# Optimization experiments

Measured on AMD Instinct MI355X. Metric: run time of the kernel, lower is better.

The kernel has to match this reference:

```python
import jax, jax.numpy as jnp
import numpy as np

B, T, H, F, K, NB, MAXL = 32, 512, 512, 512, 3, 256, 2048


def _conv1d(x, w, b, pad):
    # x: [B,T,Cin], w: [K,Cin,Cout] -> [B,T,Cout]
    y = jax.lax.conv_general_dilated(x, w, window_strides=(1,), padding=[(pad, pad)],
                                     dimension_numbers=('NWC', 'WIO', 'NWC'))
    return y + b


def _layernorm(x, g, b):
    m = jnp.mean(x, axis=-1, keepdims=True)
    v = jnp.mean((x - m) ** 2, axis=-1, keepdims=True)
    return (x - m) * jax.lax.rsqrt(v + 1e-5) * g + b


def _variance_predictor(x, mask, cw1, cb1, g1, b1, cw2, cb2, g2, b2, lw, lb, k):
    # ConvNorm(k, pad=(k-1)//2) -> ReLU -> LN -> ConvNorm(k, pad=1) -> ReLU -> LN -> Linear(F,1)
    h = _layernorm(jax.nn.relu(_conv1d(x, cw1, cb1, (k - 1) // 2)), g1, b1)
    h = _layernorm(jax.nn.relu(_conv1d(h, cw2, cb2, 1)), g2, b2)
    out = h @ lw + lb  # [B,T]
    return jnp.where(mask, 0.0, out)


def setup_inputs() -> dict:
    key = jax.random.key(0)
    ks = jax.random.split(key, 12)
    s = 0.02
    inp = {
        'x': jax.random.normal(ks[0], (B, T, H), jnp.float32),
        'src_mask': jnp.zeros((B, T), jnp.bool_),
        'duration': jax.random.randint(ks[1], (B, T), 0, 8),
        'pitch_target': jax.random.normal(ks[2], (B, T), jnp.float32),
        'energy_target': jax.random.normal(ks[3], (B, T), jnp.float32),
        # stacked predictor params: index 0=duration, 1=pitch, 2=energy
        'conv1_w': jax.random.normal(ks[4], (3, K, H, F), jnp.float32) * s,
        'conv1_b': jnp.zeros((3, F), jnp.float32),
        'ln1_g': jnp.ones((3, F), jnp.float32),
        'ln1_b': jnp.zeros((3, F), jnp.float32),
        'conv2_w': jax.random.normal(ks[5], (3, K, F, F), jnp.float32) * s,
        'conv2_b': jnp.zeros((3, F), jnp.float32),
        'ln2_g': jnp.ones((3, F), jnp.float32),
        'ln2_b': jnp.zeros((3, F), jnp.float32),
        'lin_w': jax.random.normal(ks[6], (3, F), jnp.float32) * s,
        'lin_b': jnp.zeros((3,), jnp.float32),
        'pitch_bins': jnp.linspace(-3.0, 3.0, NB - 1, dtype=jnp.float32),
        'energy_bins': jnp.linspace(-3.0, 3.0, NB - 1, dtype=jnp.float32),
        'pitch_table': jax.random.normal(ks[7], (NB, H), jnp.float32) * s,
        'energy_table': jax.random.normal(ks[8], (NB, H), jnp.float32) * s,
        'max_len': MAXL,
    }
    return inp


def reference(x, src_mask, duration, pitch_target, energy_target,
              conv1_w, conv1_b, ln1_g, ln1_b, conv2_w, conv2_b, ln2_g, ln2_b,
              lin_w, lin_b, pitch_bins, energy_bins, pitch_table, energy_table, max_len):
    k = conv1_w.shape[1]

    def vp(i, inp):
        return _variance_predictor(inp, src_mask, conv1_w[i], conv1_b[i], ln1_g[i], ln1_b[i],
                                   conv2_w[i], conv2_b[i], ln2_g[i], ln2_b[i], lin_w[i], lin_b[i], k)

    log_duration_pred = vp(0, x)
    # pitch: predict, bucketize target, add embedding (training path with targets)
    pitch_pred = vp(1, x)
    p_idx = jnp.searchsorted(pitch_bins, pitch_target)  # torch.bucketize
    x = x + pitch_table[p_idx]
    # energy on pitch-conditioned features
    energy_pred = vp(2, x)
    e_idx = jnp.searchsorted(energy_bins, energy_target)
    x = x + energy_table[e_idx]

    # LengthRegulator: expand each phoneme vec duration[b,i] times, pad to max_len
    dur = jnp.where(src_mask, 0, duration)
    cum = jnp.cumsum(dur, axis=1)                 # [B,T]
    mel_len = jnp.minimum(cum[:, -1], max_len)    # [B]
    frames = jnp.arange(max_len)
    idx = jax.vmap(lambda c: jnp.searchsorted(c, frames, side='right'))(cum)
    idx = jnp.clip(idx, 0, x.shape[1] - 1)        # [B,max_len]
    x_out = jnp.take_along_axis(x, idx[:, :, None], axis=1)  # [B,max_len,H]
    mel_mask = frames[None, :] >= mel_len[:, None]
    x_out = jnp.where(mel_mask[:, :, None], 0.0, x_out)
    return x_out, log_duration_pred, pitch_pred, energy_pred, mel_len, mel_mask
```

## Files before the change

kernel.cpp:

```cpp
#include <hip/hip_runtime.h>
#include <hip/hip_bf16.h>

typedef unsigned short ushort_t;
typedef unsigned int uint_t;
typedef __attribute__((ext_vector_type(8))) short bf16x8;
typedef __attribute__((ext_vector_type(4))) float f32x4;

#define NB_T 512
#define NB_H 512
#define NB_B 32
#define NB_M (NB_B * NB_T)
#define KDIM 1536
#define MAXL 2048

__device__ __forceinline__ ushort_t f2bf(float f) {
  __hip_bfloat16 h = __float2bfloat16(f);
  return *reinterpret_cast<ushort_t*>(&h);
}
__device__ __forceinline__ float bf2f(ushort_t u) {
  __hip_bfloat16 h;
  *reinterpret_cast<ushort_t*>(&h) = u;
  return __bfloat162float(h);
}
__device__ __forceinline__ uint_t pack2(float a, float b) {
  return (uint_t)f2bf(a) | ((uint_t)f2bf(b) << 16);
}
__device__ __forceinline__ void gload_lds16(const void* g, void* l) {
  __builtin_amdgcn_global_load_lds((const __attribute__((address_space(1))) void*)g,
                                   (__attribute__((address_space(3))) void*)l, 16, 0, 0);
}

__global__ __launch_bounds__(256) void k_wt(const float* __restrict__ w, ushort_t* __restrict__ wt) {
  __shared__ float tile[64][65];
  const int pk = blockIdx.y;
  const int p = pk / 3, kk = pk % 3;
  const int ot = (blockIdx.x & 7) * 64;
  const int it = (blockIdx.x >> 3) * 64;
  const int tx = threadIdx.x & 63;
  const int ty = threadIdx.x >> 6;
  const float* src = w + (size_t)pk * 512 * 512;
  #pragma unroll
  for (int r = ty; r < 64; r += 4)
    tile[r][tx] = src[(size_t)(it + r) * 512 + ot + tx];
  __syncthreads();
  #pragma unroll
  for (int r = ty; r < 64; r += 4)
    wt[((size_t)(p * 512 + ot + r)) * KDIM + kk * 512 + it + tx] = f2bf(tile[tx][r]);
}

__global__ __launch_bounds__(256) void k_prep_x(const float* __restrict__ x,
                                                ushort_t* __restrict__ xb_pad,
                                                ushort_t* __restrict__ ln_pad) {
  const int rp = blockIdx.x;
  const int b = rp / 514, j = rp % 514;
  const int tid = threadIdx.x;
  uint_t* dstA = (uint_t*)(xb_pad + (size_t)rp * 512);
  if (j == 0 || j == 513) {
    dstA[tid] = 0u;
    ((uint_t*)(ln_pad + (size_t)rp * 512))[tid] = 0u;
  } else {
    const float2 xv = ((const float2*)(x + ((size_t)(b * NB_T + j - 1)) * 512))[tid];
    dstA[tid] = pack2(xv.x, xv.y);
  }
}

__global__ __launch_bounds__(256) void k_bucket(const float* __restrict__ pt, const float* __restrict__ et,
                                                const float* __restrict__ pb, const float* __restrict__ eb,
                                                int* __restrict__ pi, int* __restrict__ ei) {
  const int i = blockIdx.x * 256 + threadIdx.x;
  if (i >= NB_M) return;
  float v = pt[i];
  int lo = 0, hi = 255;
  while (lo < hi) { int mid = (lo + hi) >> 1; if (pb[mid] < v) lo = mid + 1; else hi = mid; }
  pi[i] = lo;
  v = et[i]; lo = 0; hi = 255;
  while (lo < hi) { int mid = (lo + hi) >> 1; if (eb[mid] < v) lo = mid + 1; else hi = mid; }
  ei[i] = lo;
}

__global__ __launch_bounds__(512) void k_cum(const int* __restrict__ dur, const unsigned char* __restrict__ mask,
                                             int* __restrict__ cum, float* __restrict__ mel_len_out,
                                             float* __restrict__ mel_mask_out) {
  __shared__ int s[512];
  const int b = blockIdx.x, t = threadIdx.x;
  int d = mask[b * NB_T + t] ? 0 : dur[b * NB_T + t];
  s[t] = d;
  __syncthreads();
  for (int off = 1; off < 512; off <<= 1) {
    int v = (t >= off) ? s[t - off] : 0;
    __syncthreads();
    s[t] += v;
    __syncthreads();
  }
  cum[b * NB_T + t] = s[t];
  int ml = s[511]; ml = ml < MAXL ? ml : MAXL;
  if (t == 0) mel_len_out[b] = (float)ml;
  for (int f = t; f < MAXL; f += 512)
    mel_mask_out[b * MAXL + f] = (f >= ml) ? 1.0f : 0.0f;
}

__global__ __launch_bounds__(256) void k_gemm(const ushort_t* __restrict__ Apad,
                                              const ushort_t* __restrict__ Wt,
                                              const float* __restrict__ bias,
                                              ushort_t* __restrict__ H) {
  __shared__ short lA[128 * 32];
  __shared__ short lB[128 * 32];
  const int tid = threadIdx.x;
  const int lane = tid & 63, wid = tid >> 6;
  const int mt = blockIdx.x >> 2, nt = blockIdx.x & 3;
  const int m0 = mt * 128, n0 = nt * 128;
  const int b = m0 >> 9, t0 = m0 & 511;
  const long Arow0 = (long)b * 514 + t0 + 1;

  const int subr = lane >> 2;
  const int ioff = (lane & 3) * 8;

  f32x4 acc[4][4];
  #pragma unroll
  for (int i = 0; i < 4; ++i)
    #pragma unroll
    for (int j = 0; j < 4; ++j) acc[i][j] = (f32x4)0.f;

  const int wr = wid >> 1, wc = wid & 1;
  const int lr = lane & 15, kg = lane >> 4;

  for (int kk = 0; kk < 48; ++kk) {
    const int dt = (kk >> 4) - 1;
    const int i0 = (kk & 15) << 5;
    #pragma unroll
    for (int q = 0; q < 2; ++q) {
      const int chunk = wid * 2 + q;
      const int r = chunk * 16 + subr;
      const ushort_t* gsrc = Apad + (size_t)(Arow0 + r + dt) * 512 + i0 + ioff;
      gload_lds16(gsrc, &lA[chunk * 512]);
    }
    #pragma unroll
    for (int q = 0; q < 2; ++q) {
      const int chunk = wid * 2 + q;
      const int r = chunk * 16 + subr;
      const ushort_t* gsrc = Wt + (size_t)(n0 + r) * KDIM + kk * 32 + ioff;
      gload_lds16(gsrc, &lB[chunk * 512]);
    }
    __syncthreads();
    bf16x8 af[4], bfv[4];
    #pragma unroll
    for (int fi = 0; fi < 4; ++fi)
      af[fi] = *(const bf16x8*)&lA[(wr * 64 + fi * 16 + lr) * 32 + kg * 8];
    #pragma unroll
    for (int fj = 0; fj < 4; ++fj)
      bfv[fj] = *(const bf16x8*)&lB[(wc * 64 + fj * 16 + lr) * 32 + kg * 8];
    #pragma unroll
    for (int fi = 0; fi < 4; ++fi)
      #pragma unroll
      for (int fj = 0; fj < 4; ++fj)
        acc[fi][fj] = __builtin_amdgcn_mfma_f32_16x16x32_bf16(af[fi], bfv[fj], acc[fi][fj], 0, 0, 0);
    __syncthreads();
  }

  #pragma unroll
  for (int fi = 0; fi < 4; ++fi) {
    const int row = m0 + wr * 64 + fi * 16 + kg * 4;
    #pragma unroll
    for (int fj = 0; fj < 4; ++fj) {
      const int col = n0 + wc * 64 + fj * 16 + lr;
      const float bv = bias[col];
      #pragma unroll
      for (int r = 0; r < 4; ++r) {
        float v = acc[fi][fj][r] + bv;
        v = v > 0.f ? v : 0.f;
        H[(size_t)(row + r) * 512 + col] = f2bf(v);
      }
    }
  }
}

__global__ __launch_bounds__(256) void k_ln_mid(const ushort_t* __restrict__ Hh,
                                                const float* __restrict__ g, const float* __restrict__ bb,
                                                ushort_t* __restrict__ out_pad) {
  const int row = blockIdx.x * 4 + (threadIdx.x >> 6);
  const int lane = threadIdx.x & 63;
  bf16x8 v = *(const bf16x8*)(Hh + (size_t)row * 512 + lane * 8);
  float xv[8];
  float s = 0.f;
  #pragma unroll
  for (int j = 0; j < 8; ++j) { xv[j] = bf2f((ushort_t)v[j]); s += xv[j]; }
  #pragma unroll
  for (int m = 32; m >= 1; m >>= 1) s += __shfl_xor(s, m, 64);
  const float mean = s * (1.f / 512.f);
  float vs = 0.f;
  #pragma unroll
  for (int j = 0; j < 8; ++j) { float d = xv[j] - mean; vs += d * d; }
  #pragma unroll
  for (int m = 32; m >= 1; m >>= 1) vs += __shfl_xor(vs, m, 64);
  const float rstd = rsqrtf(vs * (1.f / 512.f) + 1e-5f);
  const float4 g0 = ((const float4*)(g + lane * 8))[0];
  const float4 g1 = ((const float4*)(g + lane * 8))[1];
  const float4 b0 = ((const float4*)(bb + lane * 8))[0];
  const float4 b1 = ((const float4*)(bb + lane * 8))[1];
  const float gg[8] = {g0.x, g0.y, g0.z, g0.w, g1.x, g1.y, g1.z, g1.w};
  const float bv[8] = {b0.x, b0.y, b0.z, b0.w, b1.x, b1.y, b1.z, b1.w};
  bf16x8 o;
  #pragma unroll
  for (int j = 0; j < 8; ++j) o[j] = (short)f2bf((xv[j] - mean) * rstd * gg[j] + bv[j]);
  const int bidx = row >> 9, t = row & 511;
  *(bf16x8*)(out_pad + ((size_t)(bidx * 514 + t + 1)) * 512 + lane * 8) = o;
}

__global__ __launch_bounds__(256) void k_ln_fin(const ushort_t* __restrict__ Hh,
                                                const float* __restrict__ g, const float* __restrict__ bb,
                                                const float* __restrict__ lw, const float* __restrict__ lbp,
                                                const unsigned char* __restrict__ mask,
                                                float* __restrict__ outp) {
  const int row = blockIdx.x * 4 + (threadIdx.x >> 6);
  const int lane = threadIdx.x & 63;
  bf16x8 v = *(const bf16x8*)(Hh + (size_t)row * 512 + lane * 8);
  float xv[8];
  float s = 0.f;
  #pragma unroll
  for (int j = 0; j < 8; ++j) { xv[j] = bf2f((ushort_t)v[j]); s += xv[j]; }
  #pragma unroll
  for (int m = 32; m >= 1; m >>= 1) s += __shfl_xor(s, m, 64);
  const float mean = s * (1.f / 512.f);
  float vs = 0.f;
  #pragma unroll
  for (int j = 0; j < 8; ++j) { float d = xv[j] - mean; vs += d * d; }
  #pragma unroll
  for (int m = 32; m >= 1; m >>= 1) vs += __shfl_xor(vs, m, 64);
  const float rstd = rsqrtf(vs * (1.f / 512.f) + 1e-5f);
  const float4 g0 = ((const float4*)(g + lane * 8))[0];
  const float4 g1 = ((const float4*)(g + lane * 8))[1];
  const float4 b0 = ((const float4*)(bb + lane * 8))[0];
  const float4 b1 = ((const float4*)(bb + lane * 8))[1];
  const float4 w0 = ((const float4*)(lw + lane * 8))[0];
  const float4 w1 = ((const float4*)(lw + lane * 8))[1];
  const float gg[8] = {g0.x, g0.y, g0.z, g0.w, g1.x, g1.y, g1.z, g1.w};
  const float bv[8] = {b0.x, b0.y, b0.z, b0.w, b1.x, b1.y, b1.z, b1.w};
  const float ww[8] = {w0.x, w0.y, w0.z, w0.w, w1.x, w1.y, w1.z, w1.w};
  float dot = 0.f;
  #pragma unroll
  for (int j = 0; j < 8; ++j) dot += ((xv[j] - mean) * rstd * gg[j] + bv[j]) * ww[j];
  #pragma unroll
  for (int m = 32; m >= 1; m >>= 1) dot += __shfl_xor(dot, m, 64);
  if (lane == 0) {
    float val = dot + lbp[0];
    if (mask[row]) val = 0.f;
    outp[row] = val;
  }
}

__global__ __launch_bounds__(256) void k_addemb1(const float* __restrict__ x, const float* __restrict__ tab,
                                                 const int* __restrict__ idx, float* __restrict__ x2f,
                                                 ushort_t* __restrict__ xb_pad) {
  const int m = blockIdx.x, tid = threadIdx.x;
  const int b = m >> 9, t = m & 511;
  const float2 xv = ((const float2*)(x + (size_t)m * 512))[tid];
  const float2 tv = ((const float2*)(tab + (size_t)idx[m] * 512))[tid];
  float2 r; r.x = xv.x + tv.x; r.y = xv.y + tv.y;
  ((float2*)(x2f + (size_t)m * 512))[tid] = r;
  ((uint_t*)(xb_pad + ((size_t)(b * 514 + t + 1)) * 512))[tid] = pack2(r.x, r.y);
}

__global__ __launch_bounds__(256) void k_addemb2(const float* __restrict__ tab, const int* __restrict__ idx,
                                                 float* __restrict__ x2f) {
  const int m = blockIdx.x, tid = threadIdx.x;
  const float2 tv = ((const float2*)(tab + (size_t)idx[m] * 512))[tid];
  float2 r = ((const float2*)(x2f + (size_t)m * 512))[tid];
  r.x += tv.x; r.y += tv.y;
  ((float2*)(x2f + (size_t)m * 512))[tid] = r;
}

__global__ __launch_bounds__(128) void k_regulate(const float* __restrict__ x2f, const int* __restrict__ cum,
                                                  float* __restrict__ xout) {
  const int bid = blockIdx.x;
  const int b = bid >> 11, f = bid & 2047;
  const int* c = cum + b * NB_T;
  int ml = c[511]; ml = ml < MAXL ? ml : MAXL;
  const int tid = threadIdx.x;
  float4 val = make_float4(0.f, 0.f, 0.f, 0.f);
  if (f < ml) {
    int lo = 0, hi = 512;
    while (lo < hi) { int mid = (lo + hi) >> 1; if (c[mid] <= f) lo = mid + 1; else hi = mid; }
    if (lo > 511) lo = 511;
    val = ((const float4*)(x2f + ((size_t)(b * NB_T + lo)) * 512))[tid];
  }
  ((float4*)(xout + ((size_t)(b * MAXL + f)) * 512))[tid] = val;
}

extern "C" void kernel_launch(void* const* d_in, const int* in_sizes, int n_in,
                              void* d_out, int out_size, void* d_ws, size_t ws_size,
                              hipStream_t stream) {
  const float* x        = (const float*)d_in[0];
  const unsigned char* src_mask = (const unsigned char*)d_in[1];
  const int* duration   = (const int*)d_in[2];
  const float* pitch_t  = (const float*)d_in[3];
  const float* energy_t = (const float*)d_in[4];
  const float* conv1_w  = (const float*)d_in[5];
  const float* conv1_b  = (const float*)d_in[6];
  const float* ln1_g    = (const float*)d_in[7];
  const float* ln1_b    = (const float*)d_in[8];
  const float* conv2_w  = (const float*)d_in[9];
  const float* conv2_b  = (const float*)d_in[10];
  const float* ln2_g    = (const float*)d_in[11];
  const float* ln2_b    = (const float*)d_in[12];
  const float* lin_w    = (const float*)d_in[13];
  const float* lin_b    = (const float*)d_in[14];
  const float* pbins    = (const float*)d_in[15];
  const float* ebins    = (const float*)d_in[16];
  const float* ptab     = (const float*)d_in[17];
  const float* etab     = (const float*)d_in[18];

  char* ws = (char*)d_ws;
  ushort_t* xb_pad = (ushort_t*)(ws + 0);
  ushort_t* ln_pad = (ushort_t*)(ws + 16842752);
  ushort_t* wt1    = (ushort_t*)(ws + 33685504);
  ushort_t* wt2    = (ushort_t*)(ws + 38404096);
  ushort_t* hbuf   = (ushort_t*)(ws + 43122688);
  float*    x2f    = (float*)   (ws + 59899904);
  int*      p_idx  = (int*)     (ws + 93454336);
  int*      e_idx  = (int*)     (ws + 93519872);
  int*      cum    = (int*)     (ws + 93585408);

  float* out      = (float*)d_out;
  float* o_xout   = out;
  float* o_logd   = out + 33554432;
  float* o_pitch  = o_logd + 16384;
  float* o_energy = o_pitch + 16384;
  float* o_mellen = o_energy + 16384;
  float* o_mmask  = o_mellen + 32;

  k_wt<<<dim3(64, 9), 256, 0, stream>>>(conv1_w, wt1);
  k_wt<<<dim3(64, 9), 256, 0, stream>>>(conv2_w, wt2);
  k_prep_x<<<NB_B * 514, 256, 0, stream>>>(x, xb_pad, ln_pad);
  k_bucket<<<NB_M / 256, 256, 0, stream>>>(pitch_t, energy_t, pbins, ebins, p_idx, e_idx);
  k_cum<<<NB_B, 512, 0, stream>>>(duration, src_mask, cum, o_mellen, o_mmask);

  k_gemm<<<512, 256, 0, stream>>>(xb_pad, wt1, conv1_b, hbuf);
  k_ln_mid<<<NB_M / 4, 256, 0, stream>>>(hbuf, ln1_g, ln1_b, ln_pad);
  k_gemm<<<512, 256, 0, stream>>>(ln_pad, wt2, conv2_b, hbuf);
  k_ln_fin<<<NB_M / 4, 256, 0, stream>>>(hbuf, ln2_g, ln2_b, lin_w, lin_b, src_mask, o_logd);

  k_gemm<<<512, 256, 0, stream>>>(xb_pad, wt1 + (size_t)1 * 512 * KDIM, conv1_b + 512, hbuf);
  k_ln_mid<<<NB_M / 4, 256, 0, stream>>>(hbuf, ln1_g + 512, ln1_b + 512, ln_pad);
  k_gemm<<<512, 256, 0, stream>>>(ln_pad, wt2 + (size_t)1 * 512 * KDIM, conv2_b + 512, hbuf);
  k_ln_fin<<<NB_M / 4, 256, 0, stream>>>(hbuf, ln2_g + 512, ln2_b + 512, lin_w + 512, lin_b + 1, src_mask, o_pitch);

  k_addemb1<<<NB_M, 256, 0, stream>>>(x, ptab, p_idx, x2f, xb_pad);

  k_gemm<<<512, 256, 0, stream>>>(xb_pad, wt1 + (size_t)2 * 512 * KDIM, conv1_b + 1024, hbuf);
  k_ln_mid<<<NB_M / 4, 256, 0, stream>>>(hbuf, ln1_g + 1024, ln1_b + 1024, ln_pad);
  k_gemm<<<512, 256, 0, stream>>>(ln_pad, wt2 + (size_t)2 * 512 * KDIM, conv2_b + 1024, hbuf);
  k_ln_fin<<<NB_M / 4, 256, 0, stream>>>(hbuf, ln2_g + 1024, ln2_b + 1024, lin_w + 1024, lin_b + 2, src_mask, o_energy);

  k_addemb2<<<NB_M, 256, 0, stream>>>(etab, e_idx, x2f);

  k_regulate<<<NB_B * MAXL, 128, 0, stream>>>(x2f, cum, o_xout);
}
```

Before: 573.0 us.

## Batch three predictors into single GEMM/LN launches with double-buffered LDS and staged epilogue

Runs the duration, pitch and energy predictors together. Each GEMM and LayerNorm stage becomes one launch over all three predictors instead of three sequential launches. Both embedding additions move up front into a single prep kernel that also builds the padded bf16 inputs. The GEMM now double-buffers its LDS tiles so the next K-slice load overlaps the MFMAs, remaps blocks with a swizzle, and stages its output through LDS for vectorized stores. In exchange it uses more workspace, since there are three padded input buffers and a hidden buffer three times larger, and it reuses the layer-1 input buffers in place as the layer-2 inputs.

```diff
diff --git a/kernel.cpp b/kernel.cpp
--- a/kernel.cpp
+++ b/kernel.cpp
@@ -7,11 +7,11 @@
 typedef __attribute__((ext_vector_type(4))) float f32x4;
 
 #define NB_T 512
-#define NB_H 512
 #define NB_B 32
 #define NB_M (NB_B * NB_T)
 #define KDIM 1536
 #define MAXL 2048
+#define EPI_STRIDE 144
 
 __device__ __forceinline__ ushort_t f2bf(float f) {
   __hip_bfloat16 h = __float2bfloat16(f);
@@ -46,22 +46,6 @@
   #pragma unroll
   for (int r = ty; r < 64; r += 4)
     wt[((size_t)(p * 512 + ot + r)) * KDIM + kk * 512 + it + tx] = f2bf(tile[tx][r]);
-}
-
-__global__ __launch_bounds__(256) void k_prep_x(const float* __restrict__ x,
-                                                ushort_t* __restrict__ xb_pad,
-                                                ushort_t* __restrict__ ln_pad) {
-  const int rp = blockIdx.x;
-  const int b = rp / 514, j = rp % 514;
-  const int tid = threadIdx.x;
-  uint_t* dstA = (uint_t*)(xb_pad + (size_t)rp * 512);
-  if (j == 0 || j == 513) {
-    dstA[tid] = 0u;
-    ((uint_t*)(ln_pad + (size_t)rp * 512))[tid] = 0u;
-  } else {
-    const float2 xv = ((const float2*)(x + ((size_t)(b * NB_T + j - 1)) * 512))[tid];
-    dstA[tid] = pack2(xv.x, xv.y);
-  }
 }
 
 __global__ __launch_bounds__(256) void k_bucket(const float* __restrict__ pt, const float* __restrict__ et,
@@ -99,111 +83,165 @@
     mel_mask_out[b * MAXL + f] = (f >= ml) ? 1.0f : 0.0f;
 }
 
-__global__ __launch_bounds__(256) void k_gemm(const ushort_t* __restrict__ Apad,
+__global__ __launch_bounds__(256) void k_prep(const float* __restrict__ x,
+                                              const float* __restrict__ ptab, const float* __restrict__ etab,
+                                              const int* __restrict__ pidx, const int* __restrict__ eidx,
+                                              ushort_t* __restrict__ xb_pad, ushort_t* __restrict__ x2pad,
+                                              ushort_t* __restrict__ lnp2, float* __restrict__ x3f) {
+  const int rp = blockIdx.x;
+  const int b = rp / 514, j = rp % 514;
+  const int tid = threadIdx.x;
+  if (j == 0 || j == 513) {
+    ((uint_t*)(xb_pad + (size_t)rp * 512))[tid] = 0u;
+    ((uint_t*)(x2pad + (size_t)rp * 512))[tid] = 0u;
+    ((uint_t*)(lnp2 + (size_t)rp * 512))[tid] = 0u;
+    return;
+  }
+  const int m = b * NB_T + j - 1;
+  const float2 xv = ((const float2*)(x + (size_t)m * 512))[tid];
+  const float2 pv = ((const float2*)(ptab + (size_t)pidx[m] * 512))[tid];
+  const float2 ev = ((const float2*)(etab + (size_t)eidx[m] * 512))[tid];
+  ((uint_t*)(xb_pad + (size_t)rp * 512))[tid] = pack2(xv.x, xv.y);
+  const float ax = xv.x + pv.x, ay = xv.y + pv.y;
+  ((uint_t*)(x2pad + (size_t)rp * 512))[tid] = pack2(ax, ay);
+  float2 o; o.x = ax + ev.x; o.y = ay + ev.y;
+  ((float2*)(x3f + (size_t)m * 512))[tid] = o;
+}
+
+__global__ __launch_bounds__(256) void k_gemm(const ushort_t* __restrict__ A0,
+                                              const ushort_t* __restrict__ A1,
+                                              const ushort_t* __restrict__ A2,
                                               const ushort_t* __restrict__ Wt,
                                               const float* __restrict__ bias,
                                               ushort_t* __restrict__ H) {
-  __shared__ short lA[128 * 32];
-  __shared__ short lB[128 * 32];
+  __shared__ short smem[18432];
   const int tid = threadIdx.x;
   const int lane = tid & 63, wid = tid >> 6;
-  const int mt = blockIdx.x >> 2, nt = blockIdx.x & 3;
+
+  const int h = blockIdx.x;
+  const int logical = (h & 7) * 192 + (h >> 3);
+  const int pred = logical >> 9;
+  const int tile = logical & 511;
+  const int mt = tile >> 2, nt = tile & 3;
   const int m0 = mt * 128, n0 = nt * 128;
   const int b = m0 >> 9, t0 = m0 & 511;
   const long Arow0 = (long)b * 514 + t0 + 1;
 
+  const ushort_t* Ap = (pred == 0) ? A0 : ((pred == 1) ? A1 : A2);
+  const ushort_t* Wp = Wt + (size_t)pred * 512 * KDIM;
+  const float* bp = bias + pred * 512;
+  ushort_t* Hp = H + (size_t)pred * NB_M * 512;
+
   const int subr = lane >> 2;
   const int ioff = (lane & 3) * 8;
-
-  f32x4 acc[4][4];
-  #pragma unroll
-  for (int i = 0; i < 4; ++i)
-    #pragma unroll
-    for (int j = 0; j < 4; ++j) acc[i][j] = (f32x4)0.f;
-
   const int wr = wid >> 1, wc = wid & 1;
   const int lr = lane & 15, kg = lane >> 4;
 
-  for (int kk = 0; kk < 48; ++kk) {
+  f32x4 acc[4][4];
+  #pragma unroll
+  for (int i = 0; i < 4; ++i)
+    #pragma unroll
+    for (int j = 0; j < 4; ++j) acc[i][j] = (f32x4)0.f;
+
+  auto STAGE = [&](int kk, int buf) {
     const int dt = (kk >> 4) - 1;
     const int i0 = (kk & 15) << 5;
+    short* la = &smem[buf * 8192];
+    short* lb = &smem[buf * 8192 + 4096];
     #pragma unroll
     for (int q = 0; q < 2; ++q) {
       const int chunk = wid * 2 + q;
       const int r = chunk * 16 + subr;
-      const ushort_t* gsrc = Apad + (size_t)(Arow0 + r + dt) * 512 + i0 + ioff;
-      gload_lds16(gsrc, &lA[chunk * 512]);
+      gload_lds16(Ap + (size_t)(Arow0 + r + dt) * 512 + i0 + ioff, &la[chunk * 512]);
+      gload_lds16(Wp + (size_t)(n0 + r) * KDIM + kk * 32 + ioff, &lb[chunk * 512]);
     }
-    #pragma unroll
-    for (int q = 0; q < 2; ++q) {
-      const int chunk = wid * 2 + q;
-      const int r = chunk * 16 + subr;
-      const ushort_t* gsrc = Wt + (size_t)(n0 + r) * KDIM + kk * 32 + ioff;
-      gload_lds16(gsrc, &lB[chunk * 512]);
-    }
-    __syncthreads();
+  };
+
+  STAGE(0, 0);
+  __syncthreads();
+  int buf = 0;
+  for (int kk = 0; kk < 48; ++kk) {
+    if (kk < 47) STAGE(kk + 1, buf ^ 1);
+    const short* la = &smem[buf * 8192];
+    const short* lb = &smem[buf * 8192 + 4096];
     bf16x8 af[4], bfv[4];
     #pragma unroll
     for (int fi = 0; fi < 4; ++fi)
-      af[fi] = *(const bf16x8*)&lA[(wr * 64 + fi * 16 + lr) * 32 + kg * 8];
+      af[fi] = *(const bf16x8*)&la[(wr * 64 + fi * 16 + lr) * 32 + kg * 8];
     #pragma unroll
     for (int fj = 0; fj < 4; ++fj)
-      bfv[fj] = *(const bf16x8*)&lB[(wc * 64 + fj * 16 + lr) * 32 + kg * 8];
+      bfv[fj] = *(const bf16x8*)&lb[(wc * 64 + fj * 16 + lr) * 32 + kg * 8];
     #pragma unroll
     for (int fi = 0; fi < 4; ++fi)
       #pragma unroll
       for (int fj = 0; fj < 4; ++fj)
         acc[fi][fj] = __builtin_amdgcn_mfma_f32_16x16x32_bf16(af[fi], bfv[fj], acc[fi][fj], 0, 0, 0);
     __syncthreads();
-  }
-
+    buf ^= 1;
+  }
+
+  float bvv[4];
+  #pragma unroll
+  for (int fj = 0; fj < 4; ++fj) bvv[fj] = bp[n0 + wc * 64 + fj * 16 + lr];
   #pragma unroll
   for (int fi = 0; fi < 4; ++fi) {
-    const int row = m0 + wr * 64 + fi * 16 + kg * 4;
+    const int rowb = wr * 64 + fi * 16 + kg * 4;
     #pragma unroll
     for (int fj = 0; fj < 4; ++fj) {
-      const int col = n0 + wc * 64 + fj * 16 + lr;
-      const float bv = bias[col];
+      const int col = wc * 64 + fj * 16 + lr;
       #pragma unroll
       for (int r = 0; r < 4; ++r) {
-        float v = acc[fi][fj][r] + bv;
+        float v = acc[fi][fj][r] + bvv[fj];
         v = v > 0.f ? v : 0.f;
-        H[(size_t)(row + r) * 512 + col] = f2bf(v);
+        smem[(rowb + r) * EPI_STRIDE + col] = (short)f2bf(v);
       }
     }
   }
+  __syncthreads();
+  #pragma unroll
+  for (int s = 0; s < 8; ++s) {
+    const int chunk = tid + s * 256;
+    const int row = chunk >> 4, c8 = (chunk & 15) * 8;
+    bf16x8 vv = *(const bf16x8*)&smem[row * EPI_STRIDE + c8];
+    *(bf16x8*)(Hp + (size_t)(m0 + row) * 512 + n0 + c8) = vv;
+  }
 }
 
 __global__ __launch_bounds__(256) void k_ln_mid(const ushort_t* __restrict__ Hh,
                                                 const float* __restrict__ g, const float* __restrict__ bb,
-                                                ushort_t* __restrict__ out_pad) {
-  const int row = blockIdx.x * 4 + (threadIdx.x >> 6);
+                                                ushort_t* __restrict__ lnp0, ushort_t* __restrict__ lnp1,
+                                                ushort_t* __restrict__ lnp2) {
+  const int rr = blockIdx.x * 4 + (threadIdx.x >> 6);
+  const int pred = rr >> 14, m = rr & (NB_M - 1);
   const int lane = threadIdx.x & 63;
-  bf16x8 v = *(const bf16x8*)(Hh + (size_t)row * 512 + lane * 8);
+  const float* gp = g + pred * 512;
+  const float* bp = bb + pred * 512;
+  ushort_t* dst = (pred == 0) ? lnp0 : ((pred == 1) ? lnp1 : lnp2);
+  bf16x8 v = *(const bf16x8*)(Hh + (size_t)rr * 512 + lane * 8);
   float xv[8];
   float s = 0.f;
   #pragma unroll
   for (int j = 0; j < 8; ++j) { xv[j] = bf2f((ushort_t)v[j]); s += xv[j]; }
   #pragma unroll
-  for (int m = 32; m >= 1; m >>= 1) s += __shfl_xor(s, m, 64);
+  for (int mm = 32; mm >= 1; mm >>= 1) s += __shfl_xor(s, mm, 64);
   const float mean = s * (1.f / 512.f);
   float vs = 0.f;
   #pragma unroll
   for (int j = 0; j < 8; ++j) { float d = xv[j] - mean; vs += d * d; }
   #pragma unroll
-  for (int m = 32; m >= 1; m >>= 1) vs += __shfl_xor(vs, m, 64);
+  for (int mm = 32; mm >= 1; mm >>= 1) vs += __shfl_xor(vs, mm, 64);
   const float rstd = rsqrtf(vs * (1.f / 512.f) + 1e-5f);
-  const float4 g0 = ((const float4*)(g + lane * 8))[0];
-  const float4 g1 = ((const float4*)(g + lane * 8))[1];
-  const float4 b0 = ((const float4*)(bb + lane * 8))[0];
-  const float4 b1 = ((const float4*)(bb + lane * 8))[1];
+  const float4 g0 = ((const float4*)(gp + lane * 8))[0];
+  const float4 g1 = ((const float4*)(gp + lane * 8))[1];
+  const float4 b0 = ((const float4*)(bp + lane * 8))[0];
+  const float4 b1 = ((const float4*)(bp + lane * 8))[1];
   const float gg[8] = {g0.x, g0.y, g0.z, g0.w, g1.x, g1.y, g1.z, g1.w};
   const float bv[8] = {b0.x, b0.y, b0.z, b0.w, b1.x, b1.y, b1.z, b1.w};
   bf16x8 o;
   #pragma unroll
   for (int j = 0; j < 8; ++j) o[j] = (short)f2bf((xv[j] - mean) * rstd * gg[j] + bv[j]);
-  const int bidx = row >> 9, t = row & 511;
-  *(bf16x8*)(out_pad + ((size_t)(bidx * 514 + t + 1)) * 512 + lane * 8) = o;
+  const int bidx = m >> 9, t = m & 511;
+  *(bf16x8*)(dst + ((size_t)(bidx * 514 + t + 1)) * 512 + lane * 8) = o;
 }
 
 __global__ __launch_bounds__(256) void k_ln_fin(const ushort_t* __restrict__ Hh,
@@ -211,28 +249,32 @@
                                                 const float* __restrict__ lw, const float* __restrict__ lbp,
                                                 const unsigned char* __restrict__ mask,
                                                 float* __restrict__ outp) {
-  const int row = blockIdx.x * 4 + (threadIdx.x >> 6);
+  const int rr = blockIdx.x * 4 + (threadIdx.x >> 6);
+  const int pred = rr >> 14, m = rr & (NB_M - 1);
   const int lane = threadIdx.x & 63;
-  bf16x8 v = *(const bf16x8*)(Hh + (size_t)row * 512 + lane * 8);
+  const float* gp = g + pred * 512;
+  const float* bp = bb + pred * 512;
+  const float* wp = lw + pred * 512;
+  bf16x8 v = *(const bf16x8*)(Hh + (size_t)rr * 512 + lane * 8);
   float xv[8];
   float s = 0.f;
   #pragma unroll
   for (int j = 0; j < 8; ++j) { xv[j] = bf2f((ushort_t)v[j]); s += xv[j]; }
   #pragma unroll
-  for (int m = 32; m >= 1; m >>= 1) s += __shfl_xor(s, m, 64);
+  for (int mm = 32; mm >= 1; mm >>= 1) s += __shfl_xor(s, mm, 64);
   const float mean = s * (1.f / 512.f);
   float vs = 0.f;
   #pragma unroll
   for (int j = 0; j < 8; ++j) { float d = xv[j] - mean; vs += d * d; }
   #pragma unroll
-  for (int m = 32; m >= 1; m >>= 1) vs += __shfl_xor(vs, m, 64);
+  for (int mm = 32; mm >= 1; mm >>= 1) vs += __shfl_xor(vs, mm, 64);
   const float rstd = rsqrtf(vs * (1.f / 512.f) + 1e-5f);
-  const float4 g0 = ((const float4*)(g + lane * 8))[0];
-  const float4 g1 = ((const float4*)(g + lane * 8))[1];
-  const float4 b0 = ((const float4*)(bb + lane * 8))[0];
-  const float4 b1 = ((const float4*)(bb + lane * 8))[1];
-  const float4 w0 = ((const float4*)(lw + lane * 8))[0];
-  const float4 w1 = ((const float4*)(lw + lane * 8))[1];
+  const float4 g0 = ((const float4*)(gp + lane * 8))[0];
+  const float4 g1 = ((const float4*)(gp + lane * 8))[1];
+  const float4 b0 = ((const float4*)(bp + lane * 8))[0];
+  const float4 b1 = ((const float4*)(bp + lane * 8))[1];
+  const float4 w0 = ((const float4*)(wp + lane * 8))[0];
+  const float4 w1 = ((const float4*)(wp + lane * 8))[1];
   const float gg[8] = {g0.x, g0.y, g0.z, g0.w, g1.x, g1.y, g1.z, g1.w};
   const float bv[8] = {b0.x, b0.y, b0.z, b0.w, b1.x, b1.y, b1.z, b1.w};
   const float ww[8] = {w0.x, w0.y, w0.z, w0.w, w1.x, w1.y, w1.z, w1.w};
@@ -240,36 +282,15 @@
   #pragma unroll
   for (int j = 0; j < 8; ++j) dot += ((xv[j] - mean) * rstd * gg[j] + bv[j]) * ww[j];
   #pragma unroll
-  for (int m = 32; m >= 1; m >>= 1) dot += __shfl_xor(dot, m, 64);
+  for (int mm = 32; mm >= 1; mm >>= 1) dot += __shfl_xor(dot, mm, 64);
   if (lane == 0) {
-    float val = dot + lbp[0];
-    if (mask[row]) val = 0.f;
-    outp[row] = val;
-  }
-}
-
-__global__ __launch_bounds__(256) void k_addemb1(const float* __restrict__ x, const float* __restrict__ tab,
-                                                 const int* __restrict__ idx, float* __restrict__ x2f,
-                                                 ushort_t* __restrict__ xb_pad) {
-  const int m = blockIdx.x, tid = threadIdx.x;
-  const int b = m >> 9, t = m & 511;
-  const float2 xv = ((const float2*)(x + (size_t)m * 512))[tid];
-  const float2 tv = ((const float2*)(tab + (size_t)idx[m] * 512))[tid];
-  float2 r; r.x = xv.x + tv.x; r.y = xv.y + tv.y;
-  ((float2*)(x2f + (size_t)m * 512))[tid] = r;
-  ((uint_t*)(xb_pad + ((size_t)(b * 514 + t + 1)) * 512))[tid] = pack2(r.x, r.y);
-}
-
-__global__ __launch_bounds__(256) void k_addemb2(const float* __restrict__ tab, const int* __restrict__ idx,
-                                                 float* __restrict__ x2f) {
-  const int m = blockIdx.x, tid = threadIdx.x;
-  const float2 tv = ((const float2*)(tab + (size_t)idx[m] * 512))[tid];
-  float2 r = ((const float2*)(x2f + (size_t)m * 512))[tid];
-  r.x += tv.x; r.y += tv.y;
-  ((float2*)(x2f + (size_t)m * 512))[tid] = r;
-}
-
-__global__ __launch_bounds__(128) void k_regulate(const float* __restrict__ x2f, const int* __restrict__ cum,
+    float val = dot + lbp[pred];
+    if (mask[m]) val = 0.f;
+    outp[pred * NB_M + m] = val;
+  }
+}
+
+__global__ __launch_bounds__(128) void k_regulate(const float* __restrict__ x3f, const int* __restrict__ cum,
                                                   float* __restrict__ xout) {
   const int bid = blockIdx.x;
   const int b = bid >> 11, f = bid & 2047;
@@ -281,7 +302,7 @@
     int lo = 0, hi = 512;
     while (lo < hi) { int mid = (lo + hi) >> 1; if (c[mid] <= f) lo = mid + 1; else hi = mid; }
     if (lo > 511) lo = 511;
-    val = ((const float4*)(x2f + ((size_t)(b * NB_T + lo)) * 512))[tid];
+    val = ((const float4*)(x3f + ((size_t)(b * NB_T + lo)) * 512))[tid];
   }
   ((float4*)(xout + ((size_t)(b * MAXL + f)) * 512))[tid] = val;
 }
@@ -310,48 +331,33 @@
   const float* etab     = (const float*)d_in[18];
 
   char* ws = (char*)d_ws;
-  ushort_t* xb_pad = (ushort_t*)(ws + 0);
-  ushort_t* ln_pad = (ushort_t*)(ws + 16842752);
-  ushort_t* wt1    = (ushort_t*)(ws + 33685504);
-  ushort_t* wt2    = (ushort_t*)(ws + 38404096);
-  ushort_t* hbuf   = (ushort_t*)(ws + 43122688);
-  float*    x2f    = (float*)   (ws + 59899904);
-  int*      p_idx  = (int*)     (ws + 93454336);
-  int*      e_idx  = (int*)     (ws + 93519872);
-  int*      cum    = (int*)     (ws + 93585408);
+  ushort_t* wt1    = (ushort_t*)(ws + 0);
+  ushort_t* wt2    = (ushort_t*)(ws + 4718592);
+  ushort_t* xb_pad = (ushort_t*)(ws + 9437184);
+  ushort_t* x2pad  = (ushort_t*)(ws + 26279936);
+  ushort_t* lnp2   = (ushort_t*)(ws + 43122688);
+  ushort_t* hbuf   = (ushort_t*)(ws + 59965440);
+  float*    x3f    = (float*)   (ws + 110297088);
+  int*      p_idx  = (int*)     (ws + 143851520);
+  int*      e_idx  = (int*)     (ws + 143917056);
+  int*      cum    = (int*)     (ws + 143982592);
 
   float* out      = (float*)d_out;
   float* o_xout   = out;
-  float* o_logd   = out + 33554432;
-  float* o_pitch  = o_logd + 16384;
-  float* o_energy = o_pitch + 16384;
-  float* o_mellen = o_energy + 16384;
+  float* o_preds  = out + 33554432;
+  float* o_mellen = o_preds + 3 * NB_M;
   float* o_mmask  = o_mellen + 32;
 
+  k_bucket<<<NB_M / 256, 256, 0, stream>>>(pitch_t, energy_t, pbins, ebins, p_idx, e_idx);
+  k_cum<<<NB_B, 512, 0, stream>>>(duration, src_mask, cum, o_mellen, o_mmask);
   k_wt<<<dim3(64, 9), 256, 0, stream>>>(conv1_w, wt1);
   k_wt<<<dim3(64, 9), 256, 0, stream>>>(conv2_w, wt2);
-  k_prep_x<<<NB_B * 514, 256, 0, stream>>>(x, xb_pad, ln_pad);
-  k_bucket<<<NB_M / 256, 256, 0, stream>>>(pitch_t, energy_t, pbins, ebins, p_idx, e_idx);
-  k_cum<<<NB_B, 512, 0, stream>>>(duration, src_mask, cum, o_mellen, o_mmask);
-
-  k_gemm<<<512, 256, 0, stream>>>(xb_pad, wt1, conv1_b, hbuf);
-  k_ln_mid<<<NB_M / 4, 256, 0, stream>>>(hbuf, ln1_g, ln1_b, ln_pad);
-  k_gemm<<<512, 256, 0, stream>>>(ln_pad, wt2, conv2_b, hbuf);
-  k_ln_fin<<<NB_M / 4, 256, 0, stream>>>(hbuf, ln2_g, ln2_b, lin_w, lin_b, src_mask, o_logd);
-
-  k_gemm<<<512, 256, 0, stream>>>(xb_pad, wt1 + (size_t)1 * 512 * KDIM, conv1_b + 512, hbuf);
-  k_ln_mid<<<NB_M / 4, 256, 0, stream>>>(hbuf, ln1_g + 512, ln1_b + 512, ln_pad);
-  k_gemm<<<512, 256, 0, stream>>>(ln_pad, wt2 + (size_t)1 * 512 * KDIM, conv2_b + 512, hbuf);
-  k_ln_fin<<<NB_M / 4, 256, 0, stream>>>(hbuf, ln2_g + 512, ln2_b + 512, lin_w + 512, lin_b + 1, src_mask, o_pitch);
-
-  k_addemb1<<<NB_M, 256, 0, stream>>>(x, ptab, p_idx, x2f, xb_pad);
-
-  k_gemm<<<512, 256, 0, stream>>>(xb_pad, wt1 + (size_t)2 * 512 * KDIM, conv1_b + 1024, hbuf);
-  k_ln_mid<<<NB_M / 4, 256, 0, stream>>>(hbuf, ln1_g + 1024, ln1_b + 1024, ln_pad);
-  k_gemm<<<512, 256, 0, stream>>>(ln_pad, wt2 + (size_t)2 * 512 * KDIM, conv2_b + 1024, hbuf);
-  k_ln_fin<<<NB_M / 4, 256, 0, stream>>>(hbuf, ln2_g + 1024, ln2_b + 1024, lin_w + 1024, lin_b + 2, src_mask, o_energy);
-
-  k_addemb2<<<NB_M, 256, 0, stream>>>(etab, e_idx, x2f);
-
-  k_regulate<<<NB_B * MAXL, 128, 0, stream>>>(x2f, cum, o_xout);
-}
+  k_prep<<<NB_B * 514, 256, 0, stream>>>(x, ptab, etab, p_idx, e_idx, xb_pad, x2pad, lnp2, x3f);
+
+  k_gemm<<<1536, 256, 0, stream>>>(xb_pad, xb_pad, x2pad, wt1, conv1_b, hbuf);
+  k_ln_mid<<<3 * NB_M / 4, 256, 0, stream>>>(hbuf, ln1_g, ln1_b, xb_pad, x2pad, lnp2);
+  k_gemm<<<1536, 256, 0, stream>>>(xb_pad, x2pad, lnp2, wt2, conv2_b, hbuf);
+  k_ln_fin<<<3 * NB_M / 4, 256, 0, stream>>>(hbuf, ln2_g, ln2_b, lin_w, lin_b, src_mask, o_preds);
+
+  k_regulate<<<NB_B * MAXL, 128, 0, stream>>>(x3f, cum, o_xout);
+}
```

New measurement: 503.2 us. -12.2%, faster.
